# Performance work log

Hardware: AMD Instinct MI355X
Metric: run time of the kernel (lower is better)

## Reference

```python
import jax, jax.numpy as jnp
import numpy as np

NUM_HEADS = 12
HEAD_DIM = 64
EPS = 1e-6


def _layernorm(x, g, b):
    mu = jnp.mean(x, axis=-1, keepdims=True)
    var = jnp.mean(jnp.square(x - mu), axis=-1, keepdims=True)
    return (x - mu) * jax.lax.rsqrt(var + EPS) * g + b


def setup_inputs() -> dict:
    key = jax.random.key(0)
    ks = jax.random.split(key, 8)
    D, DFF = 768, 3072
    s = lambda d: 1.0 / np.sqrt(d)
    return {
        "hidden_states": jax.random.normal(ks[0], (4, 2048, D), jnp.float32),
        "ln1_g": jnp.ones((D,), jnp.float32),
        "ln1_b": jnp.zeros((D,), jnp.float32),
        "w_qkv": jax.random.normal(ks[1], (D, 3 * D), jnp.float32) * s(D),
        "b_qkv": jnp.zeros((3 * D,), jnp.float32),
        "w_attn": jax.random.normal(ks[2], (D, D), jnp.float32) * s(D),
        "b_attn": jnp.zeros((D,), jnp.float32),
        "ln2_g": jnp.ones((D,), jnp.float32),
        "ln2_b": jnp.zeros((D,), jnp.float32),
        "w_in": jax.random.normal(ks[3], (D, DFF), jnp.float32) * s(D),
        "b_in": jnp.zeros((DFF,), jnp.float32),
        "w_out": jax.random.normal(ks[4], (DFF, D), jnp.float32) * s(DFF),
        "b_out": jnp.zeros((D,), jnp.float32),
    }


def reference(hidden_states, ln1_g, ln1_b, w_qkv, b_qkv, w_attn, b_attn,
              ln2_g, ln2_b, w_in, b_in, w_out, b_out):
    B, S, D = hidden_states.shape
    residual = hidden_states
    h = _layernorm(hidden_states, ln1_g, ln1_b)
    # QKV: [B,S,3D] -> [B,S,3,H,hd] -> [3,B,H,S,hd]
    qkv = (h @ w_qkv + b_qkv).reshape(B, S, 3, NUM_HEADS, HEAD_DIM)
    qkv = jnp.transpose(qkv, (2, 0, 3, 1, 4))
    scale = HEAD_DIM ** (-0.5)
    q, k, v = qkv[0] * scale, qkv[1], qkv[2]
    scores = jnp.einsum("bhqd,bhkd->bhqk", q, k)
    attn = jax.nn.softmax(scores, axis=-1)
    o = jnp.einsum("bhqk,bhkd->bhqd", attn, v)
    o = jnp.transpose(o, (0, 2, 1, 3)).reshape(B, S, D)
    h = residual + (o @ w_attn + b_attn)
    residual2 = h
    h2 = _layernorm(h, ln2_g, ln2_b)
    h2 = jax.nn.gelu(h2 @ w_in + b_in, approximate=False)
    h2 = h2 @ w_out + b_out
    return residual2 + h2
```

## Files before the change

kernel.cpp:

```cpp
#include <hip/hip_runtime.h>

typedef __bf16 bf16_t;
typedef bf16_t bf16x8 __attribute__((ext_vector_type(8)));
typedef float f32x4 __attribute__((ext_vector_type(4)));
typedef unsigned short ushortx8 __attribute__((ext_vector_type(8)));
typedef unsigned short ushortx4 __attribute__((ext_vector_type(4)));
typedef short short4v __attribute__((ext_vector_type(4)));

union U8 { ushortx4 h[2]; bf16x8 b; ushortx8 u; };
union SV { bf16_t h[4]; short4v s; };

__device__ __forceinline__ unsigned short f2bf(float f) {
  union { bf16_t h; unsigned short u; } cv;
  cv.h = (bf16_t)f;
  return cv.u;
}

__device__ __forceinline__ void gl_lds16(const unsigned short* g, unsigned short* l) {
  __builtin_amdgcn_global_load_lds((const __attribute__((address_space(1))) void*)g,
                                   (__attribute__((address_space(3))) void*)l,
                                   16, 0, 0);
}

__device__ __forceinline__ float gelu_fast(float v) {
  float v3 = v * v * v;
  float z = -2.30211886f * v - 0.102945f * v3;
  float e = exp2f(z);
  return v * __builtin_amdgcn_rcpf(1.0f + e);
}

__global__ __launch_bounds__(256) void ln_kernel(const float* __restrict__ x,
                                                 const float* __restrict__ g,
                                                 const float* __restrict__ b,
                                                 unsigned short* __restrict__ out) {
  int row = blockIdx.x;
  int t = threadIdx.x;
  const float* xr = x + (size_t)row * 768;
  float v0 = xr[t], v1 = xr[t + 256], v2 = xr[t + 512];
  __shared__ float red[4];
  float s = v0 + v1 + v2;
  for (int o = 32; o > 0; o >>= 1) s += __shfl_down(s, o, 64);
  if ((t & 63) == 0) red[t >> 6] = s;
  __syncthreads();
  float mu = (red[0] + red[1] + red[2] + red[3]) * (1.0f / 768.0f);
  __syncthreads();
  float d0 = v0 - mu, d1 = v1 - mu, d2 = v2 - mu;
  s = d0 * d0 + d1 * d1 + d2 * d2;
  for (int o = 32; o > 0; o >>= 1) s += __shfl_down(s, o, 64);
  if ((t & 63) == 0) red[t >> 6] = s;
  __syncthreads();
  float var = (red[0] + red[1] + red[2] + red[3]) * (1.0f / 768.0f);
  float rs = rsqrtf(var + 1e-6f);
  unsigned short* orow = out + (size_t)row * 768;
  orow[t]       = f2bf(d0 * rs * g[t]       + b[t]);
  orow[t + 256] = f2bf(d1 * rs * g[t + 256] + b[t + 256]);
  orow[t + 512] = f2bf(d2 * rs * g[t + 512] + b[t + 512]);
}

__global__ __launch_bounds__(256) void transpose_all(
    const float* __restrict__ w_qkv, const float* __restrict__ w_attn,
    const float* __restrict__ w_in, const float* __restrict__ w_out,
    unsigned short* __restrict__ wqkvT, unsigned short* __restrict__ wattnT,
    unsigned short* __restrict__ winT, unsigned short* __restrict__ woutT) {
  int id = blockIdx.x;
  const float* W; unsigned short* WT; int K, N, nx, ny;
  if (id < 1728)      { W = w_qkv;  WT = wqkvT;  K = 768;  N = 2304; nx = id % 72; ny = id / 72; }
  else if (id < 2304) { id -= 1728; W = w_attn; WT = wattnT; K = 768;  N = 768;  nx = id % 24; ny = id / 24; }
  else if (id < 4608) { id -= 2304; W = w_in;   WT = winT;   K = 768;  N = 3072; nx = id % 96; ny = id / 96; }
  else                { id -= 4608; W = w_out;  WT = woutT;  K = 3072; N = 768;  nx = id % 24; ny = id / 24; }
  __shared__ float tile[32][33];
  int n0 = nx * 32, k0 = ny * 32;
  int tx = threadIdx.x, ty = threadIdx.y;
  for (int i = 0; i < 4; i++)
    tile[ty + i * 8][tx] = W[(size_t)(k0 + ty + i * 8) * N + n0 + tx];
  __syncthreads();
  for (int i = 0; i < 4; i++)
    WT[(size_t)(n0 + ty + i * 8) * K + k0 + tx] = f2bf(tile[tx][ty + i * 8]);
}

template <int EPI, int TM>
__device__ __forceinline__ void gemm_body(const unsigned short* __restrict__ A,
                                          const unsigned short* __restrict__ BT,
                                          const float* __restrict__ bias,
                                          const float* resid,
                                          void* out, unsigned short* vt, int os,
                                          int N, int K) {
  constexpr int MI = TM / 32;
  __shared__ __align__(16) unsigned short smem[TM * 32 + 4096];
  unsigned short* As = smem;
  unsigned short* Bs = smem + TM * 32;

  int t = threadIdx.x;
  int w = t >> 6, lane = t & 63, ln = lane & 15, quad = lane >> 4;
  int wm = w & 1, wn = w >> 1;
  int m0 = blockIdx.y * TM, n0 = blockIdx.x * 128;

  int srow = w * 16 + (lane >> 2);
  int scol = (lane & 3) * 8;
  const unsigned short* gA0 = A + (size_t)(m0 + srow) * K + scol;
  const unsigned short* gA1 = gA0 + (size_t)64 * K;
  const unsigned short* gB0 = BT + (size_t)(n0 + srow) * K + scol;
  const unsigned short* gB1 = gB0 + (size_t)64 * K;
  unsigned short* dA0 = As + w * 512;
  unsigned short* dA1 = As + 2048 + w * 512;
  unsigned short* dB0 = Bs + w * 512;
  unsigned short* dB1 = Bs + 2048 + w * 512;

  f32x4 acc[MI][4];
  f32x4 zero = {0.f, 0.f, 0.f, 0.f};
  for (int mi = 0; mi < MI; mi++)
    for (int ni = 0; ni < 4; ni++) acc[mi][ni] = zero;

  int nk = K >> 5;
  for (int kt = 0; kt < nk; kt++) {
    __syncthreads();
    gl_lds16(gA0, dA0);
    if constexpr (TM == 128) gl_lds16(gA1, dA1);
    gl_lds16(gB0, dB0);
    gl_lds16(gB1, dB1);
    gA0 += 32; gA1 += 32; gB0 += 32; gB1 += 32;
    __syncthreads();
    bf16x8 af[MI], bf[4];
    for (int mi = 0; mi < MI; mi++)
      af[mi] = *(const bf16x8*)&As[(wm * (TM / 2) + mi * 16 + ln) * 32 + quad * 8];
    for (int ni = 0; ni < 4; ni++)
      bf[ni] = *(const bf16x8*)&Bs[(wn * 64 + ni * 16 + ln) * 32 + quad * 8];
    for (int mi = 0; mi < MI; mi++)
      for (int ni = 0; ni < 4; ni++)
        acc[mi][ni] = __builtin_amdgcn_mfma_f32_16x16x32_bf16(af[mi], bf[ni],
                                                              acc[mi][ni], 0, 0, 0);
  }

  if (EPI == 2) {
    float* outp = (float*)out;
    for (int mi = 0; mi < MI; mi++) {
      for (int ni = 0; ni < 4; ni++) {
        int col = n0 + wn * 64 + ni * 16 + ln;
        float bv = bias[col];
        for (int r = 0; r < 4; r++) {
          int row = m0 + wm * (TM / 2) + mi * 16 + quad * 4 + r;
          float v = acc[mi][ni][r] + bv;
          v += resid[(size_t)row * N + col];
          outp[(size_t)row * N + col] = v;
        }
      }
    }
  } else {
    __syncthreads();
    unsigned short* Cs16 = smem + w * 1024;
    unsigned short* outp = (unsigned short*)out;
    for (int mi = 0; mi < MI; mi++) {
      for (int ni = 0; ni < 4; ni++) {
        int col = n0 + wn * 64 + ni * 16 + ln;
        float bv = bias[col];
        for (int r = 0; r < 4; r++) {
          float v = acc[mi][ni][r] + bv;
          if (EPI == 0) {
            if (col < 768) v *= 0.18033688f;
          } else {
            v = gelu_fast(v);
          }
          Cs16[(quad * 4 + r) * 64 + ni * 16 + ln] = f2bf(v);
        }
      }
      __syncthreads();
      if (EPI == 0 && n0 >= 1536) {
        int c = n0 - 1536 + wn * 64 + lane;
        int s0 = m0 + wm * (TM / 2) + mi * 16;
        int bb = s0 >> 11, sl = s0 & 2047;
        ushortx8 lo, hi;
        for (int r = 0; r < 8; r++) lo[r] = Cs16[r * 64 + lane];
        for (int r = 0; r < 8; r++) hi[r] = Cs16[(8 + r) * 64 + lane];
        size_t vbase = ((size_t)(bb * 768 + c)) * 2048 + sl;
        *(ushortx8*)&vt[vbase] = lo;
        *(ushortx8*)&vt[vbase + 8] = hi;
      } else {
        int OS = (EPI == 0) ? os : N;
        for (int j = 0; j < 2; j++) {
          int rrow = j * 8 + (lane >> 3);
          int ch = (lane & 7) * 8;
          ushortx8 pv = *(const ushortx8*)&Cs16[rrow * 64 + ch];
          *(ushortx8*)&outp[(size_t)(m0 + wm * (TM / 2) + mi * 16 + rrow) * OS +
                            n0 + wn * 64 + ch] = pv;
        }
      }
      __syncthreads();
    }
  }
}

__global__ __launch_bounds__(256) void gemm_qkv(const unsigned short* A,
    const unsigned short* BT, const float* bias, void* out, unsigned short* vt,
    int N, int K) {
  gemm_body<0, 128>(A, BT, bias, nullptr, out, vt, 1536, N, K);
}
__global__ __launch_bounds__(256) void gemm_attnout(const unsigned short* A,
    const unsigned short* BT, const float* bias, const float* resid, void* out,
    int N, int K) {
  gemm_body<2, 64>(A, BT, bias, resid, out, nullptr, N, N, K);
}
__global__ __launch_bounds__(256) void gemm_ffn1(const unsigned short* A,
    const unsigned short* BT, const float* bias, void* out, int N, int K) {
  gemm_body<1, 128>(A, BT, bias, nullptr, out, nullptr, N, N, K);
}
__global__ __launch_bounds__(256) void gemm_ffn2(const unsigned short* A,
    const unsigned short* BT, const float* bias, const float* resid, void* out,
    int N, int K) {
  gemm_body<2, 64>(A, BT, bias, resid, out, nullptr, N, N, K);
}

__global__ __launch_bounds__(512, 4) void flash_attn(
    const unsigned short* __restrict__ qk, const unsigned short* __restrict__ v_t,
    unsigned short* __restrict__ o) {
  int qt = blockIdx.x;
  int bh = blockIdx.y;
  int b = bh / 12, h = bh % 12;
  int t = threadIdx.x;
  int w = t >> 6, lane = t & 63, ln = lane & 15, quad = lane >> 4;
  int qg = w & 3, kh2 = w >> 2;

  __shared__ __align__(16) unsigned short smem[18432];
  int qrow0 = b * 2048 + qt * 128;
  int qw = qrow0 + qg * 32;

  bf16x8 qf[2][2];
  for (int qi = 0; qi < 2; qi++)
    for (int kh = 0; kh < 2; kh++)
      qf[qi][kh] = *(const bf16x8*)&qk[(size_t)(qw + qi * 16 + ln) * 1536 +
                                      h * 64 + kh * 32 + quad * 8];

  SV ones;
  for (int r = 0; r < 4; r++) ones.h[r] = (bf16_t)1.0f;

  f32x4 zero = {0.f, 0.f, 0.f, 0.f};
  f32x4 o_acc[4][2];
  for (int df = 0; df < 4; df++)
    for (int qi = 0; qi < 2; qi++) o_acc[df][qi] = zero;
  f32x4 l_acc[2] = {zero, zero};

  int sr = t >> 3, sc = (t & 7) * 8;
  ushortx8 kreg = *(const ushortx8*)&qk[(size_t)(b * 2048 + sr) * 1536 + 768 + h * 64 + sc];
  ushortx8 vreg = *(const ushortx8*)&v_t[(size_t)(bh * 64 + sr) * 2048 + sc];

  for (int kt = 0; kt < 32; kt++) {
    unsigned short* Ks = smem + (kt & 1) * 9216;
    unsigned short* Vt = Ks + 4608;
    *(ushortx8*)&Ks[sr * 72 + sc] = kreg;
    *(ushortx8*)&Vt[sr * 72 + sc] = vreg;
    __syncthreads();
    if (kt < 31) {
      int krow0 = b * 2048 + (kt + 1) * 64;
      kreg = *(const ushortx8*)&qk[(size_t)(krow0 + sr) * 1536 + 768 + h * 64 + sc];
      vreg = *(const ushortx8*)&v_t[(size_t)(bh * 64 + sr) * 2048 + (kt + 1) * 64 + sc];
    }

    for (int kf = 0; kf < 2; kf++) {
      int krow = kh2 * 32 + kf * 16;
      f32x4 ST[2] = {zero, zero};
      for (int kh = 0; kh < 2; kh++) {
        bf16x8 kA = *(const bf16x8*)&Ks[(krow + ln) * 72 + kh * 32 + quad * 8];
        for (int qi = 0; qi < 2; qi++)
          ST[qi] = __builtin_amdgcn_mfma_f32_16x16x32_bf16(kA, qf[qi][kh],
                                                           ST[qi], 0, 0, 0);
      }
      short4v pT[2];
      for (int qi = 0; qi < 2; qi++) {
        SV pv;
        for (int r = 0; r < 4; r++) pv.h[r] = (bf16_t)exp2f(ST[qi][r]);
        pT[qi] = pv.s;
        l_acc[qi] = __builtin_amdgcn_mfma_f32_16x16x16bf16_1k(
            ones.s, pT[qi], l_acc[qi], 0, 0, 0);
      }
      for (int df = 0; df < 4; df++) {
        short4v vA = *(const short4v*)&Vt[(df * 16 + ln) * 72 + krow + quad * 4];
        for (int qi = 0; qi < 2; qi++)
          o_acc[df][qi] = __builtin_amdgcn_mfma_f32_16x16x16bf16_1k(
              vA, pT[qi], o_acc[df][qi], 0, 0, 0);
      }
    }
  }

  __syncthreads();
  float* fb = (float*)smem;
  float* fbl = fb + 8192;
  if (kh2 == 1) {
    for (int df = 0; df < 4; df++)
      for (int qi = 0; qi < 2; qi++)
        for (int r = 0; r < 4; r++)
          fb[qg * 2048 + (qi * 16 + ln) * 64 + df * 16 + quad * 4 + r] =
              o_acc[df][qi][r];
    if (quad == 0)
      for (int qi = 0; qi < 2; qi++)
        fbl[qg * 32 + qi * 16 + ln] = l_acc[qi][0];
  }
  __syncthreads();
  float inv[2];
  if (kh2 == 0) {
    for (int qi = 0; qi < 2; qi++) {
      float lt = l_acc[qi][0] + fbl[qg * 32 + qi * 16 + ln];
      inv[qi] = 1.0f / lt;
    }
    for (int df = 0; df < 4; df++)
      for (int qi = 0; qi < 2; qi++)
        for (int r = 0; r < 4; r++)
          o_acc[df][qi][r] += fb[qg * 2048 + (qi * 16 + ln) * 64 + df * 16 + quad * 4 + r];
  }
  __syncthreads();
  if (kh2 == 0) {
    unsigned short* Osm = smem + qg * 2304;
    for (int qi = 0; qi < 2; qi++)
      for (int df = 0; df < 4; df++)
        for (int r = 0; r < 4; r++)
          Osm[(qi * 16 + ln) * 72 + df * 16 + quad * 4 + r] =
              f2bf(o_acc[df][qi][r] * inv[qi]);
  }
  __syncthreads();
  if (kh2 == 0) {
    unsigned short* Osm = smem + qg * 2304;
    for (int p2 = 0; p2 < 4; p2++) {
      int rr = p2 * 8 + (lane >> 3);
      int ch = (lane & 7) * 8;
      ushortx8 u = *(const ushortx8*)&Osm[rr * 72 + ch];
      *(ushortx8*)&o[(size_t)(qw + rr) * 768 + h * 64 + ch] = u;
    }
  }
}

extern "C" void kernel_launch(void* const* d_in, const int* in_sizes, int n_in,
                              void* d_out, int out_size, void* d_ws, size_t ws_size,
                              hipStream_t stream) {
  const float* hidden = (const float*)d_in[0];
  const float* ln1_g  = (const float*)d_in[1];
  const float* ln1_b  = (const float*)d_in[2];
  const float* w_qkv  = (const float*)d_in[3];
  const float* b_qkv  = (const float*)d_in[4];
  const float* w_attn = (const float*)d_in[5];
  const float* b_attn = (const float*)d_in[6];
  const float* ln2_g  = (const float*)d_in[7];
  const float* ln2_b  = (const float*)d_in[8];
  const float* w_in   = (const float*)d_in[9];
  const float* b_in   = (const float*)d_in[10];
  const float* w_out  = (const float*)d_in[11];
  const float* b_out  = (const float*)d_in[12];
  float* out = (float*)d_out;

  char* ws = (char*)d_ws;
  unsigned short* wqkvT  = (unsigned short*)(ws + 0);
  unsigned short* wattnT = (unsigned short*)(ws + 3538944);
  unsigned short* winT   = (unsigned short*)(ws + 4718592);
  unsigned short* woutT  = (unsigned short*)(ws + 9437184);
  unsigned short* bufX   = (unsigned short*)(ws + 14155776);
  unsigned short* bufBig = (unsigned short*)(ws + 26738688);
  unsigned short* bufQK  = bufBig;
  unsigned short* v_t    = (unsigned short*)(ws + 26738688 + 25165824);

  transpose_all<<<6912, dim3(32, 8), 0, stream>>>(w_qkv, w_attn, w_in, w_out,
                                                  wqkvT, wattnT, winT, woutT);
  ln_kernel<<<8192, 256, 0, stream>>>(hidden, ln1_g, ln1_b, bufX);
  gemm_qkv<<<dim3(18, 64), 256, 0, stream>>>(bufX, wqkvT, b_qkv, (void*)bufQK,
                                             v_t, 2304, 768);
  flash_attn<<<dim3(16, 48), 512, 0, stream>>>(bufQK, v_t, bufX);
  gemm_attnout<<<dim3(6, 128), 256, 0, stream>>>(bufX, wattnT, b_attn, hidden,
                                                 (void*)out, 768, 768);
  ln_kernel<<<8192, 256, 0, stream>>>(out, ln2_g, ln2_b, bufX);
  gemm_ffn1<<<dim3(24, 64), 256, 0, stream>>>(bufX, winT, b_in, (void*)bufBig,
                                              3072, 768);
  gemm_ffn2<<<dim3(6, 128), 256, 0, stream>>>(bufBig, woutT, b_out, out,
                                              (void*)out, 768, 3072);
}
```

Baseline: 438.1 us.

## Double-buffer GEMM LDS tiles and tune attention inner loop

The GEMM main loop now double-buffers the A and B LDS tiles, issuing the next tile's global-to-LDS loads before computing on the current one and dropping one barrier per k-step. The attention kernel raises wave priority around its MFMA groups and uses the hardware exp2 and reciprocal intrinsics in place of the libm calls. It also pads the fp32 cross-wave reduction buffer to a row stride of 65 to avoid LDS bank conflicts. Double buffering doubles GEMM shared memory, which may lower occupancy. The fast intrinsics trade a little accuracy. With a single barrier per iteration, correctness depends on the async loads into the other buffer completing before the next barrier, which needs an explicit wait that is not visible here.

```diff
diff --git a/kernel.cpp b/kernel.cpp
--- a/kernel.cpp
+++ b/kernel.cpp
@@ -86,9 +86,8 @@
                                           void* out, unsigned short* vt, int os,
                                           int N, int K) {
   constexpr int MI = TM / 32;
-  __shared__ __align__(16) unsigned short smem[TM * 32 + 4096];
-  unsigned short* As = smem;
-  unsigned short* Bs = smem + TM * 32;
+  constexpr int ASZ = TM * 32;
+  __shared__ __align__(16) unsigned short smem[2 * ASZ + 8192];
 
   int t = threadIdx.x;
   int w = t >> 6, lane = t & 63, ln = lane & 15, quad = lane >> 4;
@@ -101,10 +100,16 @@
   const unsigned short* gA1 = gA0 + (size_t)64 * K;
   const unsigned short* gB0 = BT + (size_t)(n0 + srow) * K + scol;
   const unsigned short* gB1 = gB0 + (size_t)64 * K;
-  unsigned short* dA0 = As + w * 512;
-  unsigned short* dA1 = As + 2048 + w * 512;
-  unsigned short* dB0 = Bs + w * 512;
-  unsigned short* dB1 = Bs + 2048 + w * 512;
+
+  auto stage = [&](int buf) {
+    unsigned short* Ab = smem + buf * ASZ;
+    unsigned short* Bb = smem + 2 * ASZ + buf * 4096;
+    gl_lds16(gA0, Ab + w * 512);
+    if constexpr (TM == 128) gl_lds16(gA1, Ab + 2048 + w * 512);
+    gl_lds16(gB0, Bb + w * 512);
+    gl_lds16(gB1, Bb + 2048 + w * 512);
+    gA0 += 32; gA1 += 32; gB0 += 32; gB1 += 32;
+  };
 
   f32x4 acc[MI][4];
   f32x4 zero = {0.f, 0.f, 0.f, 0.f};
@@ -112,23 +117,23 @@
     for (int ni = 0; ni < 4; ni++) acc[mi][ni] = zero;
 
   int nk = K >> 5;
+  stage(0);
+  int cur = 0;
   for (int kt = 0; kt < nk; kt++) {
     __syncthreads();
-    gl_lds16(gA0, dA0);
-    if constexpr (TM == 128) gl_lds16(gA1, dA1);
-    gl_lds16(gB0, dB0);
-    gl_lds16(gB1, dB1);
-    gA0 += 32; gA1 += 32; gB0 += 32; gB1 += 32;
-    __syncthreads();
-    bf16x8 af[MI], bf[4];
+    if (kt + 1 < nk) stage(cur ^ 1);
+    const unsigned short* Ac = smem + cur * ASZ;
+    const unsigned short* Bc = smem + 2 * ASZ + cur * 4096;
+    bf16x8 af[MI], bfr[4];
     for (int mi = 0; mi < MI; mi++)
-      af[mi] = *(const bf16x8*)&As[(wm * (TM / 2) + mi * 16 + ln) * 32 + quad * 8];
+      af[mi] = *(const bf16x8*)&Ac[(wm * (TM / 2) + mi * 16 + ln) * 32 + quad * 8];
     for (int ni = 0; ni < 4; ni++)
-      bf[ni] = *(const bf16x8*)&Bs[(wn * 64 + ni * 16 + ln) * 32 + quad * 8];
+      bfr[ni] = *(const bf16x8*)&Bc[(wn * 64 + ni * 16 + ln) * 32 + quad * 8];
     for (int mi = 0; mi < MI; mi++)
       for (int ni = 0; ni < 4; ni++)
-        acc[mi][ni] = __builtin_amdgcn_mfma_f32_16x16x32_bf16(af[mi], bf[ni],
+        acc[mi][ni] = __builtin_amdgcn_mfma_f32_16x16x32_bf16(af[mi], bfr[ni],
                                                               acc[mi][ni], 0, 0, 0);
+    cur ^= 1;
   }
 
   if (EPI == 2) {
@@ -257,37 +262,43 @@
     for (int kf = 0; kf < 2; kf++) {
       int krow = kh2 * 32 + kf * 16;
       f32x4 ST[2] = {zero, zero};
-      for (int kh = 0; kh < 2; kh++) {
-        bf16x8 kA = *(const bf16x8*)&Ks[(krow + ln) * 72 + kh * 32 + quad * 8];
-        for (int qi = 0; qi < 2; qi++)
-          ST[qi] = __builtin_amdgcn_mfma_f32_16x16x32_bf16(kA, qf[qi][kh],
-                                                           ST[qi], 0, 0, 0);
-      }
+      bf16x8 kA0 = *(const bf16x8*)&Ks[(krow + ln) * 72 + quad * 8];
+      bf16x8 kA1 = *(const bf16x8*)&Ks[(krow + ln) * 72 + 32 + quad * 8];
+      __builtin_amdgcn_s_setprio(1);
+      for (int qi = 0; qi < 2; qi++) {
+        ST[qi] = __builtin_amdgcn_mfma_f32_16x16x32_bf16(kA0, qf[qi][0], ST[qi], 0, 0, 0);
+        ST[qi] = __builtin_amdgcn_mfma_f32_16x16x32_bf16(kA1, qf[qi][1], ST[qi], 0, 0, 0);
+      }
+      __builtin_amdgcn_s_setprio(0);
       short4v pT[2];
       for (int qi = 0; qi < 2; qi++) {
         SV pv;
-        for (int r = 0; r < 4; r++) pv.h[r] = (bf16_t)exp2f(ST[qi][r]);
+        for (int r = 0; r < 4; r++)
+          pv.h[r] = (bf16_t)__builtin_amdgcn_exp2f(ST[qi][r]);
         pT[qi] = pv.s;
+      }
+      __builtin_amdgcn_s_setprio(1);
+      for (int qi = 0; qi < 2; qi++)
         l_acc[qi] = __builtin_amdgcn_mfma_f32_16x16x16bf16_1k(
             ones.s, pT[qi], l_acc[qi], 0, 0, 0);
-      }
       for (int df = 0; df < 4; df++) {
         short4v vA = *(const short4v*)&Vt[(df * 16 + ln) * 72 + krow + quad * 4];
         for (int qi = 0; qi < 2; qi++)
           o_acc[df][qi] = __builtin_amdgcn_mfma_f32_16x16x16bf16_1k(
               vA, pT[qi], o_acc[df][qi], 0, 0, 0);
       }
+      __builtin_amdgcn_s_setprio(0);
     }
   }
 
   __syncthreads();
   float* fb = (float*)smem;
-  float* fbl = fb + 8192;
+  float* fbl = fb + 8320;
   if (kh2 == 1) {
     for (int df = 0; df < 4; df++)
       for (int qi = 0; qi < 2; qi++)
         for (int r = 0; r < 4; r++)
-          fb[qg * 2048 + (qi * 16 + ln) * 64 + df * 16 + quad * 4 + r] =
+          fb[qg * 2080 + (qi * 16 + ln) * 65 + df * 16 + quad * 4 + r] =
               o_acc[df][qi][r];
     if (quad == 0)
       for (int qi = 0; qi < 2; qi++)
@@ -298,12 +309,12 @@
   if (kh2 == 0) {
     for (int qi = 0; qi < 2; qi++) {
       float lt = l_acc[qi][0] + fbl[qg * 32 + qi * 16 + ln];
-      inv[qi] = 1.0f / lt;
+      inv[qi] = __builtin_amdgcn_rcpf(lt);
     }
     for (int df = 0; df < 4; df++)
       for (int qi = 0; qi < 2; qi++)
         for (int r = 0; r < 4; r++)
-          o_acc[df][qi][r] += fb[qg * 2048 + (qi * 16 + ln) * 64 + df * 16 + quad * 4 + r];
+          o_acc[df][qi][r] += fb[qg * 2080 + (qi * 16 + ln) * 65 + df * 16 + quad * 4 + r];
   }
   __syncthreads();
   if (kh2 == 0) {
```

New measurement: 409.3 us. 1.07x faster.
